# Kernel optimization log

Hardware: AMD Instinct MI355X
Metric: run time of the kernel (lower is better)

The kernel has to match this reference:

```python
import jax, jax.numpy as jnp
import numpy as np

B, N, D = 2, 2048, 768
HEADS, DIM_HEAD = 12, 64
INNER = HEADS * DIM_HEAD  # 768
OUT_DIM = 768


def setup_inputs() -> dict:
    key = jax.random.key(0)
    k1, k2, k3, k4, k5 = jax.random.split(key, 5)
    s_in = 1.0 / np.sqrt(D)
    s_inner = 1.0 / np.sqrt(INNER)
    return {
        "x": jax.random.normal(k1, (B, N, D), dtype=jnp.float32),
        "w_qkv": jax.random.normal(k2, (D, 3 * INNER), dtype=jnp.float32) * s_in,
        "b_qkv": jax.random.normal(k3, (3 * INNER,), dtype=jnp.float32) * 0.01,
        "w_out": jax.random.normal(k4, (INNER, OUT_DIM), dtype=jnp.float32) * s_inner,
        "b_out": jax.random.normal(k5, (OUT_DIM,), dtype=jnp.float32) * 0.01,
    }


def reference(x, w_qkv, b_qkv, w_out, b_out):
    b, n, _ = x.shape
    scale = DIM_HEAD ** -0.5
    qkv = x @ w_qkv + b_qkv                      # [b, n, 3*inner]
    q, k, v = jnp.split(qkv, 3, axis=-1)
    # 'b n (h d) -> b h n d'
    reshape = lambda t: t.reshape(b, n, HEADS, DIM_HEAD).transpose(0, 2, 1, 3)
    q, k, v = reshape(q), reshape(k), reshape(v)
    dots = jnp.einsum("bhnd,bhmd->bhnm", q, k) * scale
    attn = jax.nn.softmax(dots, axis=-1)
    out = jnp.einsum("bhnm,bhmd->bhnd", attn, v)  # [b, h, n, d]
    out = out.transpose(0, 2, 1, 3).reshape(b, n, INNER)
    return out @ w_out + b_out
```

## Files before the change

### kernel.cpp

```cpp
#include <hip/hip_runtime.h>
#include <hip/hip_bf16.h>
#include <stdint.h>


typedef __attribute__((ext_vector_type(8))) short bf16x8;
typedef __attribute__((ext_vector_type(4))) float f32x4;
typedef __attribute__((address_space(3))) unsigned int lds_uint;
typedef __attribute__((address_space(1))) const unsigned int g_uint;

__device__ __forceinline__ short f2bf(float f) {
    union { float f; uint32_t u; } x; x.f = f;
    uint32_t r = (x.u + 0x7fffu + ((x.u >> 16) & 1u)) >> 16;
    return (short)r;
}
__device__ __forceinline__ uint32_t packbf(float a, float b) {
    union { float f; uint32_t u; } xa, xb; xa.f = a; xb.f = b;
    return __builtin_amdgcn_perm(xb.u + 0x8000u, xa.u + 0x8000u, 0x07060302u);
}
__device__ __forceinline__ float exp2fast(float x) {
#if __has_builtin(__builtin_amdgcn_exp2f)
    return __builtin_amdgcn_exp2f(x);
#else
    return __expf(x * 0.6931471805599453f);
#endif
}
__device__ __forceinline__ void gl_lds16(const void* g, void* l) {
    __builtin_amdgcn_global_load_lds((g_uint*)g, (lds_uint*)l, 16, 0, 0);
}

__device__ __forceinline__ void tr_tile(const float* __restrict__ W,
                                        short* __restrict__ Wt, int K, int N,
                                        int n0, int k0, int t, short* S) {
    {
        int kl = t >> 2, ng = t & 3;
        const float* src = W + (size_t)(k0 + kl) * N + n0 + ng * 16;
        #pragma unroll
        for (int j = 0; j < 16; j += 4) {
            float4 f = *(const float4*)(src + j);
            S[(ng*16 + j + 0) * 65 + kl] = f2bf(f.x);
            S[(ng*16 + j + 1) * 65 + kl] = f2bf(f.y);
            S[(ng*16 + j + 2) * 65 + kl] = f2bf(f.z);
            S[(ng*16 + j + 3) * 65 + kl] = f2bf(f.w);
        }
    }
    __syncthreads();
    {
        int nl = t >> 2, kg = t & 3;
        short* dst = Wt + (size_t)(n0 + nl) * K + k0 + kg * 16;
        #pragma unroll
        for (int j = 0; j < 16; j += 4) {
            short4 s4;
            s4.x = S[nl*65 + kg*16 + j + 0];
            s4.y = S[nl*65 + kg*16 + j + 1];
            s4.z = S[nl*65 + kg*16 + j + 2];
            s4.w = S[nl*65 + kg*16 + j + 3];
            *(short4*)(dst + j) = s4;
        }
    }
}

__global__ __launch_bounds__(256)
void prep_k(const float* __restrict__ x, short* __restrict__ Xb,
            const float* __restrict__ Wq, short* __restrict__ Wqt,
            const float* __restrict__ Wo, short* __restrict__ Wot)
{
    __shared__ short S[64 * 65];
    const int t = threadIdx.x;
    if (blockIdx.x < 1536) {
        int i = (blockIdx.x * 256 + t) * 8;
        float4 f0 = *(const float4*)(x + i);
        float4 f1 = *(const float4*)(x + i + 4);
        short s[8];
        s[0]=f2bf(f0.x); s[1]=f2bf(f0.y); s[2]=f2bf(f0.z); s[3]=f2bf(f0.w);
        s[4]=f2bf(f1.x); s[5]=f2bf(f1.y); s[6]=f2bf(f1.z); s[7]=f2bf(f1.w);
        *(uint4*)(Xb + i) = *(uint4*)s;
        return;
    }
    if (blockIdx.x < 1968) {
        const int b2 = blockIdx.x - 1536;
        tr_tile(Wq, Wqt, 768, 2304, (b2 % 36) * 64, (b2 / 36) * 64, t, S);
    } else {
        const int b3 = blockIdx.x - 1968;
        tr_tile(Wo, Wot, 768, 768, (b3 % 12) * 64, (b3 / 12) * 64, t, S);
    }
}

__global__ __launch_bounds__(256)
void tr_w(const float* __restrict__ W, short* __restrict__ Wt, int K, int N) {
    __shared__ short S[64 * 65];
    tr_tile(W, Wt, K, N, blockIdx.x * 64, blockIdx.y * 64, threadIdx.x, S);
}

__global__ __launch_bounds__(256)
void gemm_qkv(const short* __restrict__ A, const short* __restrict__ Bt,
              const float* __restrict__ bias,
              short* __restrict__ Qb, short* __restrict__ Kb, short* __restrict__ Vt)
{
    __shared__ short As[128 * 32];
    __shared__ short Bs[96 * 32];
    const int tid = threadIdx.x, lane = tid & 63, w = tid >> 6;
    const int wm = w >> 1, wn = w & 1, quad = lane >> 4, lcol = lane & 15;
    const int bm = blockIdx.y * 128, bn = blockIdx.x * 96;

    f32x4 acc[4][3];
    #pragma unroll
    for (int i = 0; i < 4; i++)
        #pragma unroll
        for (int j = 0; j < 3; j++) acc[i][j] = (f32x4){0.f, 0.f, 0.f, 0.f};

    for (int kt = 0; kt < 768; kt += 32) {
        #pragma unroll
        for (int i = 0; i < 2; i++) {
            int c = tid + i * 256, row = c >> 2, cs = c & 3;
            gl_lds16(A + (size_t)(bm + row) * 768 + kt + cs * 8, As + c * 8);
        }
        {
            int c = tid, row = c >> 2, cs = c & 3;
            gl_lds16(Bt + (size_t)(bn + row) * 768 + kt + cs * 8, Bs + c * 8);
        }
        if (tid < 128) {
            int c = 256 + tid, row = c >> 2, cs = c & 3;
            gl_lds16(Bt + (size_t)(bn + row) * 768 + kt + cs * 8, Bs + c * 8);
        }
        __syncthreads();
        bf16x8 a[4], b[3];
        #pragma unroll
        for (int tm = 0; tm < 4; tm++)
            a[tm] = *(const bf16x8*)(As + (wm*64 + tm*16 + lcol) * 32 + quad * 8);
        #pragma unroll
        for (int tn = 0; tn < 3; tn++)
            b[tn] = *(const bf16x8*)(Bs + (wn*48 + tn*16 + lcol) * 32 + quad * 8);
        #pragma unroll
        for (int tm = 0; tm < 4; tm++)
            #pragma unroll
            for (int tn = 0; tn < 3; tn++)
                acc[tm][tn] = __builtin_amdgcn_mfma_f32_16x16x32_bf16(a[tm], b[tn], acc[tm][tn], 0, 0, 0);
        __syncthreads();
    }

    const float SCLQ = 0.18033688011112042f;
    #pragma unroll
    for (int tm = 0; tm < 4; tm++) {
        #pragma unroll
        for (int tn = 0; tn < 3; tn++) {
            int col = bn + wn*48 + tn*16 + lcol;
            float bv = bias[col];
            int which = (col >= 1536) ? 2 : (col >= 768 ? 1 : 0);
            int cc = col - which * 768;
            int h = cc >> 6, d = cc & 63;
            int rowbase = bm + wm*64 + tm*16 + quad*4;
            int bb = rowbase >> 11, n0 = rowbase & 2047;
            int bh = bb * 12 + h;
            if (which == 2) {
                short4 s4;
                s4.x = f2bf(acc[tm][tn][0] + bv);
                s4.y = f2bf(acc[tm][tn][1] + bv);
                s4.z = f2bf(acc[tm][tn][2] + bv);
                s4.w = f2bf(acc[tm][tn][3] + bv);
                *(short4*)(Vt + (((size_t)bh*32 + (n0 >> 6))*64 + d)*64 + (n0 & 63)) = s4;
            } else {
                #pragma unroll
                for (int reg = 0; reg < 4; reg++) {
                    float v = acc[tm][tn][reg] + bv;
                    if (which == 0) v *= SCLQ;
                    short* dst = (which == 0) ? Qb : Kb;
                    dst[((size_t)bh*2048 + n0 + reg)*64 + d] = f2bf(v);
                }
            }
        }
    }
}

__global__ __launch_bounds__(256)
void attn_k(const short* __restrict__ Q, const short* __restrict__ K,
            const short* __restrict__ Vt, short* __restrict__ Ab)
{
    __shared__ short Ks[2][4096];
    __shared__ short Vs[2][4096];
    __shared__ short Ps[64 * 72];
    __shared__ float lsum[64];

    const int tid = threadIdx.x, lane = tid & 63, w = tid >> 6;
    const int quad = lane >> 4, lcol = lane & 15;
    const int bid = blockIdx.x;
    const int bh = bid % 24, qt = bid / 24;
    const int b = bh / 12, h = bh - b * 12;

    const short* Kg = K  + (size_t)bh * 131072;
    const short* Vg = Vt + (size_t)bh * 131072;

    bf16x8 qf[4][2];
    {
        const short* Qg = Q + ((size_t)bh * 2048 + (size_t)qt * 64) * 64;
        #pragma unroll
        for (int qs = 0; qs < 4; qs++)
            #pragma unroll
            for (int ks = 0; ks < 2; ks++)
                qf[qs][ks] = *(const bf16x8*)(Qg + (qs*16 + lcol) * 64 + ks*32 + quad*8);
    }

    if (tid < 64) lsum[tid] = 0.f;
    #pragma unroll
    for (int i = 0; i < 2; i++) {
        int c = tid + i * 256, row = c >> 3, cs = c & 7, gc = cs ^ (row & 7);
        gl_lds16(Kg + row * 64 + gc * 8, Ks[0] + c * 8);
        gl_lds16(Vg + row * 64 + gc * 8, Vs[0] + c * 8);
    }
    __syncthreads();

    f32x4 o[4];
    #pragma unroll
    for (int tn = 0; tn < 4; tn++) o[tn] = (f32x4){0.f, 0.f, 0.f, 0.f};
    float lp[4] = {0.f, 0.f, 0.f, 0.f};

    const int krow = w * 16 + lcol;
    const int ksw  = krow & 7;

    for (int kt = 0; kt < 32; kt++) {
        const int p = kt & 1;
        if (kt < 31) {
            #pragma unroll
            for (int i = 0; i < 2; i++) {
                int c = tid + i * 256, row = c >> 3, cs = c & 7, gc = cs ^ (row & 7);
                gl_lds16(Kg + (kt + 1) * 4096 + row * 64 + gc * 8, Ks[p ^ 1] + c * 8);
                gl_lds16(Vg + (kt + 1) * 4096 + row * 64 + gc * 8, Vs[p ^ 1] + c * 8);
            }
        }

        f32x4 st[4];
        #pragma unroll
        for (int qs = 0; qs < 4; qs++) st[qs] = (f32x4){0.f, 0.f, 0.f, 0.f};
        #pragma unroll
        for (int ks = 0; ks < 2; ks++) {
            bf16x8 kf = *(const bf16x8*)(Ks[p] + krow * 64 + (((ks*4 + quad) ^ ksw) << 3));
            #pragma unroll
            for (int qs = 0; qs < 4; qs++)
                st[qs] = __builtin_amdgcn_mfma_f32_16x16x32_bf16(kf, qf[qs][ks], st[qs], 0, 0, 0);
        }

        #pragma unroll
        for (int qs = 0; qs < 4; qs++) {
            float p0 = exp2fast(st[qs][0]), p1 = exp2fast(st[qs][1]);
            float p2 = exp2fast(st[qs][2]), p3 = exp2fast(st[qs][3]);
            lp[qs] += (p0 + p1) + (p2 + p3);
            uint32_t uu[2] = { packbf(p0, p1), packbf(p2, p3) };
            *(uint32_t*)(Ps + (qs*16 + lcol) * 72 + w*16 + quad*4)     = uu[0];
            *(uint32_t*)(Ps + (qs*16 + lcol) * 72 + w*16 + quad*4 + 2) = uu[1];
        }
        __syncthreads();

        #pragma unroll
        for (int ks = 0; ks < 2; ks++) {
            bf16x8 ap = *(const bf16x8*)(Ps + (w*16 + lcol) * 72 + ks * 32 + quad * 8);
            #pragma unroll
            for (int tn = 0; tn < 4; tn++) {
                int row = tn * 16 + lcol;
                bf16x8 bv = *(const bf16x8*)(Vs[p] + row * 64 +
                                             (((ks * 4 + quad) ^ (row & 7)) << 3));
                o[tn] = __builtin_amdgcn_mfma_f32_16x16x32_bf16(ap, bv, o[tn], 0, 0, 0);
            }
        }
        __syncthreads();
    }

    #pragma unroll
    for (int qs = 0; qs < 4; qs++) {
        float v = lp[qs];
        v += __shfl_xor(v, 16, 64);
        v += __shfl_xor(v, 32, 64);
        if (quad == 0) atomicAdd(&lsum[qs*16 + lcol], v);
    }
    __syncthreads();
    #pragma unroll
    for (int tn = 0; tn < 4; tn++) {
        #pragma unroll
        for (int r = 0; r < 4; r++) {
            int q = qt * 64 + w * 16 + quad * 4 + r;
            int d = h * 64 + tn * 16 + lcol;
            float rl = 1.0f / lsum[w * 16 + quad * 4 + r];
            Ab[((size_t)(b * 2048 + q)) * 768 + d] = f2bf(o[tn][r] * rl);
        }
    }
}

__global__ __launch_bounds__(256)
void gemm_out(const short* __restrict__ A, const short* __restrict__ Bt,
              const float* __restrict__ bias, float* __restrict__ Of)
{
    __shared__ short As[64 * 32];
    __shared__ short Bs[96 * 32];
    const int tid = threadIdx.x, lane = tid & 63, w = tid >> 6;
    const int wm = w >> 1, wn = w & 1, quad = lane >> 4, lcol = lane & 15;
    const int bm = blockIdx.y * 64, bn = blockIdx.x * 96;

    f32x4 acc[2][3];
    #pragma unroll
    for (int i = 0; i < 2; i++)
        #pragma unroll
        for (int j = 0; j < 3; j++) acc[i][j] = (f32x4){0.f, 0.f, 0.f, 0.f};

    for (int kt = 0; kt < 768; kt += 32) {
        {
            int row = tid >> 2, cs = tid & 3;
            gl_lds16(A  + (size_t)(bm + row) * 768 + kt + cs * 8, As + tid * 8);
            gl_lds16(Bt + (size_t)(bn + row) * 768 + kt + cs * 8, Bs + tid * 8);
        }
        if (tid < 128) {
            int c = 256 + tid, row = c >> 2, cs = c & 3;
            gl_lds16(Bt + (size_t)(bn + row) * 768 + kt + cs * 8, Bs + c * 8);
        }
        __syncthreads();
        bf16x8 a[2], b[3];
        #pragma unroll
        for (int tm = 0; tm < 2; tm++)
            a[tm] = *(const bf16x8*)(As + (wm*32 + tm*16 + lcol) * 32 + quad * 8);
        #pragma unroll
        for (int tn = 0; tn < 3; tn++)
            b[tn] = *(const bf16x8*)(Bs + (wn*48 + tn*16 + lcol) * 32 + quad * 8);
        #pragma unroll
        for (int tm = 0; tm < 2; tm++)
            #pragma unroll
            for (int tn = 0; tn < 3; tn++)
                acc[tm][tn] = __builtin_amdgcn_mfma_f32_16x16x32_bf16(a[tm], b[tn], acc[tm][tn], 0, 0, 0);
        __syncthreads();
    }
    #pragma unroll
    for (int tm = 0; tm < 2; tm++) {
        #pragma unroll
        for (int tn = 0; tn < 3; tn++) {
            int col = bn + wn*48 + tn*16 + lcol;
            float bv = bias[col];
            #pragma unroll
            for (int reg = 0; reg < 4; reg++) {
                int row = bm + wm*32 + tm*16 + quad*4 + reg;
                Of[(size_t)row * 768 + col] = acc[tm][tn][reg] + bv;
            }
        }
    }
}

extern "C" void kernel_launch(void* const* d_in, const int* in_sizes, int n_in,
                              void* d_out, int out_size, void* d_ws, size_t ws_size,
                              hipStream_t stream)
{
    (void)in_sizes; (void)n_in; (void)out_size;
    const float* x     = (const float*)d_in[0];
    const float* w_qkv = (const float*)d_in[1];
    const float* b_qkv = (const float*)d_in[2];
    const float* w_out = (const float*)d_in[3];
    const float* b_out = (const float*)d_in[4];
    float* out = (float*)d_out;

    const size_t XSZ = (size_t)4096 * 768;
    const size_t WQ  = (size_t)2304 * 768;
    const size_t WO  = (size_t)768 * 768;
    const size_t HSZ = (size_t)24 * 2048 * 64;
    short* Xb  = (short*)d_ws;
    short* Wqt = Xb + XSZ;
    short* Qb  = Wqt + WQ;
    short* Kb  = Qb + HSZ;
    short* Vt  = Kb + HSZ;
    short* Ab  = Xb;

    const bool sepWot = ws_size >= (XSZ + WQ + 3*HSZ + WO) * sizeof(short);
    short* Wot = sepWot ? (Vt + HSZ) : Wqt;

    if (sepWot) {
        prep_k<<<2112, 256, 0, stream>>>(x, Xb, w_qkv, Wqt, w_out, Wot);
        gemm_qkv<<<dim3(24, 32), 256, 0, stream>>>(Xb, Wqt, b_qkv, Qb, Kb, Vt);
    } else {
        prep_k<<<1968, 256, 0, stream>>>(x, Xb, w_qkv, Wqt, w_out, Wot);
        gemm_qkv<<<dim3(24, 32), 256, 0, stream>>>(Xb, Wqt, b_qkv, Qb, Kb, Vt);
        tr_w<<<dim3(12, 12), 256, 0, stream>>>(w_out, Wot, 768, 768);
    }
    attn_k<<<768, 256, 0, stream>>>(Qb, Kb, Vt, Ab);
    gemm_out<<<dim3(8, 64), 256, 0, stream>>>(Ab, Wot, b_out, out);
}
```

Measured before the change: 175.1 us.

## Fuse fp32-to-bf16 conversion and weight transpose into GEMM tile loads

Drops the separate prep kernel that converted x and the weights to bf16 and transposed the weights. The QKV and output GEMMs now read fp32 inputs directly, convert them to bf16 while staging into LDS, and transpose the weight tiles there using a padded 40-element row stride. This removes one launch and the round trip through workspace memory. In exchange, every GEMM tile reloads and reconverts fp32 data, doubling global read bytes, and the weight tiles are written to LDS as scattered 2-byte stores instead of async global-to-LDS copies.

```diff
diff --git a/kernel.cpp b/kernel.cpp
--- a/kernel.cpp
+++ b/kernel.cpp
@@ -28,76 +28,13 @@
     __builtin_amdgcn_global_load_lds((g_uint*)g, (lds_uint*)l, 16, 0, 0);
 }
 
-__device__ __forceinline__ void tr_tile(const float* __restrict__ W,
-                                        short* __restrict__ Wt, int K, int N,
-                                        int n0, int k0, int t, short* S) {
-    {
-        int kl = t >> 2, ng = t & 3;
-        const float* src = W + (size_t)(k0 + kl) * N + n0 + ng * 16;
-        #pragma unroll
-        for (int j = 0; j < 16; j += 4) {
-            float4 f = *(const float4*)(src + j);
-            S[(ng*16 + j + 0) * 65 + kl] = f2bf(f.x);
-            S[(ng*16 + j + 1) * 65 + kl] = f2bf(f.y);
-            S[(ng*16 + j + 2) * 65 + kl] = f2bf(f.z);
-            S[(ng*16 + j + 3) * 65 + kl] = f2bf(f.w);
-        }
-    }
-    __syncthreads();
-    {
-        int nl = t >> 2, kg = t & 3;
-        short* dst = Wt + (size_t)(n0 + nl) * K + k0 + kg * 16;
-        #pragma unroll
-        for (int j = 0; j < 16; j += 4) {
-            short4 s4;
-            s4.x = S[nl*65 + kg*16 + j + 0];
-            s4.y = S[nl*65 + kg*16 + j + 1];
-            s4.z = S[nl*65 + kg*16 + j + 2];
-            s4.w = S[nl*65 + kg*16 + j + 3];
-            *(short4*)(dst + j) = s4;
-        }
-    }
-}
-
 __global__ __launch_bounds__(256)
-void prep_k(const float* __restrict__ x, short* __restrict__ Xb,
-            const float* __restrict__ Wq, short* __restrict__ Wqt,
-            const float* __restrict__ Wo, short* __restrict__ Wot)
-{
-    __shared__ short S[64 * 65];
-    const int t = threadIdx.x;
-    if (blockIdx.x < 1536) {
-        int i = (blockIdx.x * 256 + t) * 8;
-        float4 f0 = *(const float4*)(x + i);
-        float4 f1 = *(const float4*)(x + i + 4);
-        short s[8];
-        s[0]=f2bf(f0.x); s[1]=f2bf(f0.y); s[2]=f2bf(f0.z); s[3]=f2bf(f0.w);
-        s[4]=f2bf(f1.x); s[5]=f2bf(f1.y); s[6]=f2bf(f1.z); s[7]=f2bf(f1.w);
-        *(uint4*)(Xb + i) = *(uint4*)s;
-        return;
-    }
-    if (blockIdx.x < 1968) {
-        const int b2 = blockIdx.x - 1536;
-        tr_tile(Wq, Wqt, 768, 2304, (b2 % 36) * 64, (b2 / 36) * 64, t, S);
-    } else {
-        const int b3 = blockIdx.x - 1968;
-        tr_tile(Wo, Wot, 768, 768, (b3 % 12) * 64, (b3 / 12) * 64, t, S);
-    }
-}
-
-__global__ __launch_bounds__(256)
-void tr_w(const float* __restrict__ W, short* __restrict__ Wt, int K, int N) {
-    __shared__ short S[64 * 65];
-    tr_tile(W, Wt, K, N, blockIdx.x * 64, blockIdx.y * 64, threadIdx.x, S);
-}
-
-__global__ __launch_bounds__(256)
-void gemm_qkv(const short* __restrict__ A, const short* __restrict__ Bt,
+void gemm_qkv(const float* __restrict__ X, const float* __restrict__ Wq,
               const float* __restrict__ bias,
               short* __restrict__ Qb, short* __restrict__ Kb, short* __restrict__ Vt)
 {
-    __shared__ short As[128 * 32];
-    __shared__ short Bs[96 * 32];
+    __shared__ short As[128 * 40];
+    __shared__ short Bs[96 * 40];
     const int tid = threadIdx.x, lane = tid & 63, w = tid >> 6;
     const int wm = w >> 1, wn = w & 1, quad = lane >> 4, lcol = lane & 15;
     const int bm = blockIdx.y * 128, bn = blockIdx.x * 96;
@@ -110,26 +47,32 @@
 
     for (int kt = 0; kt < 768; kt += 32) {
         #pragma unroll
-        for (int i = 0; i < 2; i++) {
-            int c = tid + i * 256, row = c >> 2, cs = c & 3;
-            gl_lds16(A + (size_t)(bm + row) * 768 + kt + cs * 8, As + c * 8);
-        }
-        {
-            int c = tid, row = c >> 2, cs = c & 3;
-            gl_lds16(Bt + (size_t)(bn + row) * 768 + kt + cs * 8, Bs + c * 8);
-        }
-        if (tid < 128) {
-            int c = 256 + tid, row = c >> 2, cs = c & 3;
-            gl_lds16(Bt + (size_t)(bn + row) * 768 + kt + cs * 8, Bs + c * 8);
+        for (int i = 0; i < 4; i++) {
+            int fi = tid + i * 256;
+            int r = fi >> 3, c = (fi & 7) << 2;
+            float4 f = *(const float4*)(X + (size_t)(bm + r) * 768 + kt + c);
+            short4 s;
+            s.x = f2bf(f.x); s.y = f2bf(f.y); s.z = f2bf(f.z); s.w = f2bf(f.w);
+            *(short4*)(As + r * 40 + c) = s;
+        }
+        #pragma unroll
+        for (int j = 0; j < 3; j++) {
+            int fi = tid + j * 256;
+            int kr = fi & 31, ng = fi >> 5;
+            float4 f = *(const float4*)(Wq + (size_t)(kt + kr) * 2304 + bn + ng * 4);
+            Bs[(ng * 4 + 0) * 40 + kr] = f2bf(f.x);
+            Bs[(ng * 4 + 1) * 40 + kr] = f2bf(f.y);
+            Bs[(ng * 4 + 2) * 40 + kr] = f2bf(f.z);
+            Bs[(ng * 4 + 3) * 40 + kr] = f2bf(f.w);
         }
         __syncthreads();
         bf16x8 a[4], b[3];
         #pragma unroll
         for (int tm = 0; tm < 4; tm++)
-            a[tm] = *(const bf16x8*)(As + (wm*64 + tm*16 + lcol) * 32 + quad * 8);
+            a[tm] = *(const bf16x8*)(As + (wm*64 + tm*16 + lcol) * 40 + quad * 8);
         #pragma unroll
         for (int tn = 0; tn < 3; tn++)
-            b[tn] = *(const bf16x8*)(Bs + (wn*48 + tn*16 + lcol) * 32 + quad * 8);
+            b[tn] = *(const bf16x8*)(Bs + (wn*48 + tn*16 + lcol) * 40 + quad * 8);
         #pragma unroll
         for (int tm = 0; tm < 4; tm++)
             #pragma unroll
@@ -284,11 +227,11 @@
 }
 
 __global__ __launch_bounds__(256)
-void gemm_out(const short* __restrict__ A, const short* __restrict__ Bt,
+void gemm_out(const short* __restrict__ A, const float* __restrict__ Wo,
               const float* __restrict__ bias, float* __restrict__ Of)
 {
     __shared__ short As[64 * 32];
-    __shared__ short Bs[96 * 32];
+    __shared__ short Bs[96 * 40];
     const int tid = threadIdx.x, lane = tid & 63, w = tid >> 6;
     const int wm = w >> 1, wn = w & 1, quad = lane >> 4, lcol = lane & 15;
     const int bm = blockIdx.y * 64, bn = blockIdx.x * 96;
@@ -302,12 +245,17 @@
     for (int kt = 0; kt < 768; kt += 32) {
         {
             int row = tid >> 2, cs = tid & 3;
-            gl_lds16(A  + (size_t)(bm + row) * 768 + kt + cs * 8, As + tid * 8);
-            gl_lds16(Bt + (size_t)(bn + row) * 768 + kt + cs * 8, Bs + tid * 8);
-        }
-        if (tid < 128) {
-            int c = 256 + tid, row = c >> 2, cs = c & 3;
-            gl_lds16(Bt + (size_t)(bn + row) * 768 + kt + cs * 8, Bs + c * 8);
+            gl_lds16(A + (size_t)(bm + row) * 768 + kt + cs * 8, As + tid * 8);
+        }
+        #pragma unroll
+        for (int j = 0; j < 3; j++) {
+            int fi = tid + j * 256;
+            int kr = fi & 31, ng = fi >> 5;
+            float4 f = *(const float4*)(Wo + (size_t)(kt + kr) * 768 + bn + ng * 4);
+            Bs[(ng * 4 + 0) * 40 + kr] = f2bf(f.x);
+            Bs[(ng * 4 + 1) * 40 + kr] = f2bf(f.y);
+            Bs[(ng * 4 + 2) * 40 + kr] = f2bf(f.z);
+            Bs[(ng * 4 + 3) * 40 + kr] = f2bf(f.w);
         }
         __syncthreads();
         bf16x8 a[2], b[3];
@@ -316,7 +264,7 @@
             a[tm] = *(const bf16x8*)(As + (wm*32 + tm*16 + lcol) * 32 + quad * 8);
         #pragma unroll
         for (int tn = 0; tn < 3; tn++)
-            b[tn] = *(const bf16x8*)(Bs + (wn*48 + tn*16 + lcol) * 32 + quad * 8);
+            b[tn] = *(const bf16x8*)(Bs + (wn*48 + tn*16 + lcol) * 40 + quad * 8);
         #pragma unroll
         for (int tm = 0; tm < 2; tm++)
             #pragma unroll
@@ -343,7 +291,7 @@
                               void* d_out, int out_size, void* d_ws, size_t ws_size,
                               hipStream_t stream)
 {
-    (void)in_sizes; (void)n_in; (void)out_size;
+    (void)in_sizes; (void)n_in; (void)out_size; (void)ws_size;
     const float* x     = (const float*)d_in[0];
     const float* w_qkv = (const float*)d_in[1];
     const float* b_qkv = (const float*)d_in[2];
@@ -351,28 +299,13 @@
     const float* b_out = (const float*)d_in[4];
     float* out = (float*)d_out;
 
-    const size_t XSZ = (size_t)4096 * 768;
-    const size_t WQ  = (size_t)2304 * 768;
-    const size_t WO  = (size_t)768 * 768;
     const size_t HSZ = (size_t)24 * 2048 * 64;
-    short* Xb  = (short*)d_ws;
-    short* Wqt = Xb + XSZ;
-    short* Qb  = Wqt + WQ;
-    short* Kb  = Qb + HSZ;
-    short* Vt  = Kb + HSZ;
-    short* Ab  = Xb;
-
-    const bool sepWot = ws_size >= (XSZ + WQ + 3*HSZ + WO) * sizeof(short);
-    short* Wot = sepWot ? (Vt + HSZ) : Wqt;
-
-    if (sepWot) {
-        prep_k<<<2112, 256, 0, stream>>>(x, Xb, w_qkv, Wqt, w_out, Wot);
-        gemm_qkv<<<dim3(24, 32), 256, 0, stream>>>(Xb, Wqt, b_qkv, Qb, Kb, Vt);
-    } else {
-        prep_k<<<1968, 256, 0, stream>>>(x, Xb, w_qkv, Wqt, w_out, Wot);
-        gemm_qkv<<<dim3(24, 32), 256, 0, stream>>>(Xb, Wqt, b_qkv, Qb, Kb, Vt);
-        tr_w<<<dim3(12, 12), 256, 0, stream>>>(w_out, Wot, 768, 768);
-    }
+    short* Qb = (short*)d_ws;
+    short* Kb = Qb + HSZ;
+    short* Vt = Kb + HSZ;
+    short* Ab = Vt + HSZ;
+
+    gemm_qkv<<<dim3(24, 32), 256, 0, stream>>>(x, w_qkv, b_qkv, Qb, Kb, Vt);
     attn_k<<<768, 256, 0, stream>>>(Qb, Kb, Vt, Ab);
-    gemm_out<<<dim3(8, 64), 256, 0, stream>>>(Ab, Wot, b_out, out);
-}
+    gemm_out<<<dim3(8, 64), 256, 0, stream>>>(Ab, w_out, b_out, out);
+}
```

After: 193.4 us. 10.5% more time.

## Double-buffer LDS tiles in QKV and output projection GEMMs

Applied to the files above, without the earlier changes.

Both projection GEMMs now use two LDS buffers per operand. The next K-slice is issued with global-to-LDS loads before the MFMAs on the current slice run, which drops one barrier per iteration and lets memory latency overlap compute. The cost is double the LDS footprint, which may lower occupancy. Correctness depends on the async loads being complete before the single remaining barrier.

```diff
diff --git a/kernel.cpp b/kernel.cpp
--- a/kernel.cpp
+++ b/kernel.cpp
@@ -96,8 +96,8 @@
               const float* __restrict__ bias,
               short* __restrict__ Qb, short* __restrict__ Kb, short* __restrict__ Vt)
 {
-    __shared__ short As[128 * 32];
-    __shared__ short Bs[96 * 32];
+    __shared__ short As[2][128 * 32];
+    __shared__ short Bs[2][96 * 32];
     const int tid = threadIdx.x, lane = tid & 63, w = tid >> 6;
     const int wm = w >> 1, wn = w & 1, quad = lane >> 4, lcol = lane & 15;
     const int bm = blockIdx.y * 128, bn = blockIdx.x * 96;
@@ -108,28 +108,44 @@
         #pragma unroll
         for (int j = 0; j < 3; j++) acc[i][j] = (f32x4){0.f, 0.f, 0.f, 0.f};
 
-    for (int kt = 0; kt < 768; kt += 32) {
+    {
         #pragma unroll
         for (int i = 0; i < 2; i++) {
             int c = tid + i * 256, row = c >> 2, cs = c & 3;
-            gl_lds16(A + (size_t)(bm + row) * 768 + kt + cs * 8, As + c * 8);
-        }
-        {
+            gl_lds16(A + (size_t)(bm + row) * 768 + cs * 8, As[0] + c * 8);
+        }
+        int c = tid, row = c >> 2, cs = c & 3;
+        gl_lds16(Bt + (size_t)(bn + row) * 768 + cs * 8, Bs[0] + c * 8);
+        if (tid < 128) {
+            int c2 = 256 + tid, row2 = c2 >> 2, cs2 = c2 & 3;
+            gl_lds16(Bt + (size_t)(bn + row2) * 768 + cs2 * 8, Bs[0] + c2 * 8);
+        }
+    }
+    __syncthreads();
+
+    for (int it = 0; it < 24; it++) {
+        const int p = it & 1;
+        if (it < 23) {
+            int kt = (it + 1) * 32;
+            #pragma unroll
+            for (int i = 0; i < 2; i++) {
+                int c = tid + i * 256, row = c >> 2, cs = c & 3;
+                gl_lds16(A + (size_t)(bm + row) * 768 + kt + cs * 8, As[p ^ 1] + c * 8);
+            }
             int c = tid, row = c >> 2, cs = c & 3;
-            gl_lds16(Bt + (size_t)(bn + row) * 768 + kt + cs * 8, Bs + c * 8);
-        }
-        if (tid < 128) {
-            int c = 256 + tid, row = c >> 2, cs = c & 3;
-            gl_lds16(Bt + (size_t)(bn + row) * 768 + kt + cs * 8, Bs + c * 8);
-        }
-        __syncthreads();
+            gl_lds16(Bt + (size_t)(bn + row) * 768 + kt + cs * 8, Bs[p ^ 1] + c * 8);
+            if (tid < 128) {
+                int c2 = 256 + tid, row2 = c2 >> 2, cs2 = c2 & 3;
+                gl_lds16(Bt + (size_t)(bn + row2) * 768 + kt + cs2 * 8, Bs[p ^ 1] + c2 * 8);
+            }
+        }
         bf16x8 a[4], b[3];
         #pragma unroll
         for (int tm = 0; tm < 4; tm++)
-            a[tm] = *(const bf16x8*)(As + (wm*64 + tm*16 + lcol) * 32 + quad * 8);
+            a[tm] = *(const bf16x8*)(As[p] + (wm*64 + tm*16 + lcol) * 32 + quad * 8);
         #pragma unroll
         for (int tn = 0; tn < 3; tn++)
-            b[tn] = *(const bf16x8*)(Bs + (wn*48 + tn*16 + lcol) * 32 + quad * 8);
+            b[tn] = *(const bf16x8*)(Bs[p] + (wn*48 + tn*16 + lcol) * 32 + quad * 8);
         #pragma unroll
         for (int tm = 0; tm < 4; tm++)
             #pragma unroll
@@ -287,8 +303,8 @@
 void gemm_out(const short* __restrict__ A, const short* __restrict__ Bt,
               const float* __restrict__ bias, float* __restrict__ Of)
 {
-    __shared__ short As[64 * 32];
-    __shared__ short Bs[96 * 32];
+    __shared__ short As[2][64 * 32];
+    __shared__ short Bs[2][96 * 32];
     const int tid = threadIdx.x, lane = tid & 63, w = tid >> 6;
     const int wm = w >> 1, wn = w & 1, quad = lane >> 4, lcol = lane & 15;
     const int bm = blockIdx.y * 64, bn = blockIdx.x * 96;
@@ -299,24 +315,36 @@
         #pragma unroll
         for (int j = 0; j < 3; j++) acc[i][j] = (f32x4){0.f, 0.f, 0.f, 0.f};
 
-    for (int kt = 0; kt < 768; kt += 32) {
-        {
+    {
+        int row = tid >> 2, cs = tid & 3;
+        gl_lds16(A  + (size_t)(bm + row) * 768 + cs * 8, As[0] + tid * 8);
+        gl_lds16(Bt + (size_t)(bn + row) * 768 + cs * 8, Bs[0] + tid * 8);
+        if (tid < 128) {
+            int c = 256 + tid, row2 = c >> 2, cs2 = c & 3;
+            gl_lds16(Bt + (size_t)(bn + row2) * 768 + cs2 * 8, Bs[0] + c * 8);
+        }
+    }
+    __syncthreads();
+
+    for (int it = 0; it < 24; it++) {
+        const int p = it & 1;
+        if (it < 23) {
+            int kt = (it + 1) * 32;
             int row = tid >> 2, cs = tid & 3;
-            gl_lds16(A  + (size_t)(bm + row) * 768 + kt + cs * 8, As + tid * 8);
-            gl_lds16(Bt + (size_t)(bn + row) * 768 + kt + cs * 8, Bs + tid * 8);
-        }
-        if (tid < 128) {
-            int c = 256 + tid, row = c >> 2, cs = c & 3;
-            gl_lds16(Bt + (size_t)(bn + row) * 768 + kt + cs * 8, Bs + c * 8);
-        }
-        __syncthreads();
+            gl_lds16(A  + (size_t)(bm + row) * 768 + kt + cs * 8, As[p ^ 1] + tid * 8);
+            gl_lds16(Bt + (size_t)(bn + row) * 768 + kt + cs * 8, Bs[p ^ 1] + tid * 8);
+            if (tid < 128) {
+                int c = 256 + tid, row2 = c >> 2, cs2 = c & 3;
+                gl_lds16(Bt + (size_t)(bn + row2) * 768 + kt + cs2 * 8, Bs[p ^ 1] + c * 8);
+            }
+        }
         bf16x8 a[2], b[3];
         #pragma unroll
         for (int tm = 0; tm < 2; tm++)
-            a[tm] = *(const bf16x8*)(As + (wm*32 + tm*16 + lcol) * 32 + quad * 8);
+            a[tm] = *(const bf16x8*)(As[p] + (wm*32 + tm*16 + lcol) * 32 + quad * 8);
         #pragma unroll
         for (int tn = 0; tn < 3; tn++)
-            b[tn] = *(const bf16x8*)(Bs + (wn*48 + tn*16 + lcol) * 32 + quad * 8);
+            b[tn] = *(const bf16x8*)(Bs[p] + (wn*48 + tn*16 + lcol) * 32 + quad * 8);
         #pragma unroll
         for (int tm = 0; tm < 2; tm++)
             #pragma unroll
```

Result: faster. 164.3 us (-6.1%).
